# Kernel optimization log

Measured on AMD Instinct MI355X. Metric: run time of the kernel, lower is better.

Reference implementation:

```python
import jax, jax.numpy as jnp
import numpy as np

B, T, S, D, H, FF = 4, 1024, 1024, 1024, 16, 4096
DH = D // H
NEG = -1e9
EPS = 1e-5


def setup_inputs() -> dict:
    key = jax.random.key(0)
    ks = jax.random.split(key, 20)
    p = 0.02  # param init scale
    inp = {
        "x": jax.random.normal(ks[0], (B, T, D), jnp.float32),
        "encoder_output": jax.random.normal(ks[1], (B, S, D), jnp.float32),
        "src_mask": jnp.ones((B, 1, 1, S), jnp.bool_),
        "tgt_mask": jnp.tril(jnp.ones((1, 1, T, T), jnp.bool_)),  # causal
        # self-attention params
        "d_Wq": jax.random.normal(ks[2], (D, D)) * p, "d_bq": jnp.zeros((D,)),
        "d_Wk": jax.random.normal(ks[3], (D, D)) * p, "d_bk": jnp.zeros((D,)),
        "d_Wv": jax.random.normal(ks[4], (D, D)) * p, "d_bv": jnp.zeros((D,)),
        "d_Wo": jax.random.normal(ks[5], (D, D)) * p, "d_bo": jnp.zeros((D,)),
        # cross-attention params
        "e_Wq": jax.random.normal(ks[6], (D, D)) * p, "e_bq": jnp.zeros((D,)),
        "e_Wk": jax.random.normal(ks[7], (D, D)) * p, "e_bk": jnp.zeros((D,)),
        "e_Wv": jax.random.normal(ks[8], (D, D)) * p, "e_bv": jnp.zeros((D,)),
        "e_Wo": jax.random.normal(ks[9], (D, D)) * p, "e_bo": jnp.zeros((D,)),
        # FFN params
        "ff_W1": jax.random.normal(ks[10], (D, FF)) * p, "ff_b1": jnp.zeros((FF,)),
        "ff_W2": jax.random.normal(ks[11], (FF, D)) * p, "ff_b2": jnp.zeros((D,)),
        # layernorm params
        "ln1_g": jnp.ones((D,)), "ln1_b": jnp.zeros((D,)),
        "ln2_g": jnp.ones((D,)), "ln2_b": jnp.zeros((D,)),
        "ln3_g": jnp.ones((D,)), "ln3_b": jnp.zeros((D,)),
    }
    return inp


def _mha(xq, xkv, Wq, bq, Wk, bk, Wv, bv, Wo, bo, mask):
    b, tq = xq.shape[0], xq.shape[1]
    q = (xq @ Wq + bq).reshape(b, tq, H, DH).transpose(0, 2, 1, 3)
    k = (xkv @ Wk + bk).reshape(b, -1, H, DH).transpose(0, 2, 1, 3)
    v = (xkv @ Wv + bv).reshape(b, -1, H, DH).transpose(0, 2, 1, 3)
    scores = jnp.einsum("bhqd,bhkd->bhqk", q, k) / np.float32(np.sqrt(DH))
    scores = jnp.where(mask, scores, NEG)
    attn = jax.nn.softmax(scores, axis=-1)
    out = jnp.einsum("bhqk,bhkd->bhqd", attn, v)
    out = out.transpose(0, 2, 1, 3).reshape(b, tq, D)
    return out @ Wo + bo


def _ln(x, g, b):
    m = jnp.mean(x, axis=-1, keepdims=True)
    v = jnp.var(x, axis=-1, keepdims=True)
    return (x - m) / jnp.sqrt(v + EPS) * g + b


def reference(x, encoder_output, src_mask, tgt_mask,
              d_Wq, d_bq, d_Wk, d_bk, d_Wv, d_bv, d_Wo, d_bo,
              e_Wq, e_bq, e_Wk, e_bk, e_Wv, e_bv, e_Wo, e_bo,
              ff_W1, ff_b1, ff_W2, ff_b2,
              ln1_g, ln1_b, ln2_g, ln2_b, ln3_g, ln3_b):
    # masked self-attention + residual + LN (dropout is identity in eval)
    d = _mha(x, x, d_Wq, d_bq, d_Wk, d_bk, d_Wv, d_bv, d_Wo, d_bo, tgt_mask)
    d = _ln(d + x, ln1_g, ln1_b)
    # cross-attention over encoder output + residual + LN
    f = _mha(d, encoder_output, e_Wq, e_bq, e_Wk, e_bk, e_Wv, e_bv, e_Wo, e_bo, src_mask)
    f = _ln(f + d, ln2_g, ln2_b)
    # FFN + residual + LN
    g = jax.nn.relu(f @ ff_W1 + ff_b1) @ ff_W2 + ff_b2
    g = _ln(g + f, ln3_g, ln3_b)
    return g
```

## Files before the change

kernel.cpp:

```cpp
#include <hip/hip_runtime.h>

static constexpr int Bc = 4, Tc = 1024, Sc = 1024, Dc = 1024, Hc = 16, DHc = 64, FFc = 4096;

typedef __attribute__((ext_vector_type(8))) short short8;
typedef __attribute__((ext_vector_type(4))) short short4v;
typedef __attribute__((ext_vector_type(4))) float f32x4;

__device__ __forceinline__ unsigned short f2bf(float f) {
    unsigned int u = __float_as_uint(f);
    unsigned int r = u + 0x7fffu + ((u >> 16) & 1u);
    return (unsigned short)(r >> 16);
}
__device__ __forceinline__ float bf2f(unsigned short u) {
    return __uint_as_float(((unsigned int)u) << 16);
}
__device__ __forceinline__ float fexp2(float x) {
    float r; asm("v_exp_f32 %0, %1" : "=v"(r) : "v"(x)); return r;
}
__device__ __forceinline__ unsigned int cvtpk(float a, float b) {
    unsigned int r;
    asm("v_cvt_pk_bf16_f32 %0, %1, %2" : "=v"(r) : "v"(a), "v"(b));
    return r;
}

__device__ __forceinline__ void gload_lds16(const void* g, void* l) {
    __builtin_amdgcn_global_load_lds((const __attribute__((address_space(1))) void*)g,
                                     (__attribute__((address_space(3))) void*)l, 16, 0, 0);
}

__global__ __launch_bounds__(256) void cast_f32_bf16(const float* __restrict__ in,
                                                     unsigned short* __restrict__ out, int n8) {
    int i = blockIdx.x * 256 + threadIdx.x;
    if (i >= n8) return;
    const float4* p = (const float4*)in + (size_t)i * 2;
    float4 a = p[0], b = p[1];
    short8 o;
    o[0] = f2bf(a.x); o[1] = f2bf(a.y); o[2] = f2bf(a.z); o[3] = f2bf(a.w);
    o[4] = f2bf(b.x); o[5] = f2bf(b.y); o[6] = f2bf(b.z); o[7] = f2bf(b.w);
    *(short8*)(out + (size_t)i * 8) = o;
}

__global__ __launch_bounds__(256) void transpose_cast(const float* __restrict__ W,
                                                      unsigned short* __restrict__ Wt,
                                                      int K, int N) {
    __shared__ float tile[32][33];
    int n0 = blockIdx.x * 32, k0 = blockIdx.y * 32;
    int tx = threadIdx.x, ty = threadIdx.y;
#pragma unroll
    for (int i = 0; i < 4; i++)
        tile[ty + i * 8][tx] = W[(size_t)(k0 + ty + i * 8) * N + n0 + tx];
    __syncthreads();
#pragma unroll
    for (int i = 0; i < 4; i++)
        Wt[(size_t)(n0 + ty + i * 8) * K + k0 + tx] = f2bf(tile[tx][ty + i * 8]);
}

struct TP8 { const float* s[8]; unsigned short* d[8]; };
__global__ __launch_bounds__(256) void transpose_cast8(TP8 p) {
    __shared__ float tile[32][33];
    const float* W = p.s[blockIdx.z];
    unsigned short* Wt = p.d[blockIdx.z];
    int n0 = blockIdx.x * 32, k0 = blockIdx.y * 32;
    int tx = threadIdx.x, ty = threadIdx.y;
#pragma unroll
    for (int i = 0; i < 4; i++)
        tile[ty + i * 8][tx] = W[(size_t)(k0 + ty + i * 8) * 1024 + n0 + tx];
    __syncthreads();
#pragma unroll
    for (int i = 0; i < 4; i++)
        Wt[(size_t)(n0 + ty + i * 8) * 1024 + k0 + tx] = f2bf(tile[tx][ty + i * 8]);
}

__global__ void concat_bias(const float* b0, const float* b1, const float* b2,
                            float* __restrict__ out) {
    int i = blockIdx.x * 256 + threadIdx.x;
    int seg = i >> 10, j = i & 1023;
    const float* p = seg == 0 ? b0 : (seg == 1 ? b1 : b2);
    out[i] = p[j];
}

__global__ __launch_bounds__(256) void transpose_v(const unsigned short* __restrict__ V, int ldv,
                                                   unsigned short* __restrict__ Vt) {
    __shared__ unsigned short t[64 * 64];
    const int bh = blockIdx.y, b = bh >> 4, h = bh & 15;
    const int s0 = blockIdx.x * 64;
    const int tid = threadIdx.x;
    const int r = tid >> 2, ch = tid & 3;
    const unsigned short* src = V + (size_t)(b * 1024 + s0 + r) * ldv + h * 64 + ch * 16;
    short8 v0 = *(const short8*)src;
    short8 v1 = *(const short8*)(src + 8);
    int pw_ = (ch ^ r ^ (r >> 4)) & 3;
    *(short8*)(t + r * 64 + pw_ * 16) = v0;
    *(short8*)(t + r * 64 + pw_ * 16 + 8) = v1;
    __syncthreads();
    const int dh = tid >> 2, sc = (tid & 3) * 16;
    short8 o0, o1;
#pragma unroll
    for (int j = 0; j < 8; j++) {
        int c0 = sc + j, c1 = sc + 8 + j;
        o0[j] = t[c0 * 64 + (((dh >> 4) ^ c0 ^ (c0 >> 4)) & 3) * 16 + (dh & 15)];
        o1[j] = t[c1 * 64 + (((dh >> 4) ^ c1 ^ (c1 >> 4)) & 3) * 16 + (dh & 15)];
    }
    unsigned short* dst = Vt + ((size_t)bh * 64 + dh) * 1024 + s0 + sc;
    *(short8*)dst = o0;
    *(short8*)(dst + 8) = o1;
}

struct BlkMap { int m, n, z; };
__device__ __forceinline__ BlkMap remap_block() {
    const int gx = gridDim.x, gy = gridDim.y;
    const int nxy = gx * gy;
    const int nwg = nxy * gridDim.z;
    const int flat = (blockIdx.z * gy + blockIdx.y) * gx + blockIdx.x;
    const int id = (flat & 7) * (nwg >> 3) + (flat >> 3);
    const int pz = id / nxy;
    const int rz = id - pz * nxy;
    const int gwsh = (gx & 7) ? 2 : 3;
    const int gw = 1 << gwsh;
    const int gsz = gw * gy;
    const int grp = rz / gsz;
    const int rem = rz - grp * gsz;
    BlkMap r;
    r.m = rem >> gwsh;
    r.n = (grp << gwsh) + (rem & (gw - 1));
    r.z = pz;
    return r;
}

template <int EPI>
__global__ __launch_bounds__(512, 2) void gemm256(const unsigned short* __restrict__ A,
                                                  const unsigned short* __restrict__ Bt,
                                                  const float* __restrict__ bias,
                                                  unsigned short* __restrict__ outB,
                                                  int N, int lda, int ldb, int nk) {
    __shared__ unsigned short sm[4][16384];
    const int tid = threadIdx.x;
    const int lane = tid & 63, wid = tid >> 6;
    const int l4 = lane & 15, g = lane >> 4;
    const int wr = wid >> 2, wc = wid & 3;
    BlkMap bm = remap_block();
    const int m0 = bm.m * 256, n0 = bm.n * 256, z = bm.z;
    A += (size_t)z * (nk * 64);
    Bt += (size_t)z * (nk * 64);
    const int srow = tid >> 3;
    const int schunk = (tid & 7) ^ (srow & 7);
    const int sw = l4 & 7;

    auto stA = [&](int sb, int seg, int k0) {
        gload_lds16(A + (size_t)(m0 + seg * 64 + srow) * lda + k0 + schunk * 8,
                    (char*)sm[sb] + seg * 8192 + tid * 16);
    };
    auto stB = [&](int sb, int seg, int k0) {
        gload_lds16(Bt + (size_t)(n0 + seg * 64 + srow) * ldb + k0 + schunk * 8,
                    (char*)sm[2 + sb] + seg * 8192 + tid * 16);
    };

    f32x4 acc[8][4] = {};
#pragma unroll
    for (int s = 0; s < 4; s++) stB(0, s, 0);
#pragma unroll
    for (int s = 0; s < 4; s++) stA(0, s, 0);
    asm volatile("s_waitcnt vmcnt(0)" ::: "memory");
    __builtin_amdgcn_s_barrier();

    for (int t = 0; t < nk; ++t) {
        const int bufR = t & 1, bufW = bufR ^ 1;
        const int kn = (t + 1) * 64;
        const bool pf = (t + 1 < nk);
        const unsigned short* As_ = sm[bufR];
        const unsigned short* Bs_ = sm[2 + bufR];
        short8 a[4], b0[4], b1[4];
        if (pf) { stB(bufW, 0, kn); stB(bufW, 1, kn); }
#pragma unroll
        for (int n = 0; n < 4; n++)
            b0[n] = *(const short8*)(Bs_ + (wc * 64 + n * 16 + l4) * 64 + (g ^ sw) * 8);
#pragma unroll
        for (int m = 0; m < 4; m++)
            a[m] = *(const short8*)(As_ + (wr * 128 + m * 16 + l4) * 64 + (g ^ sw) * 8);
        __builtin_amdgcn_s_barrier();
        __builtin_amdgcn_s_setprio(1);
#pragma unroll
        for (int m = 0; m < 4; m++)
#pragma unroll
            for (int n = 0; n < 4; n++)
                acc[m][n] = __builtin_amdgcn_mfma_f32_16x16x32_bf16(a[m], b0[n], acc[m][n], 0, 0, 0);
        __builtin_amdgcn_s_setprio(0);
        __builtin_amdgcn_s_barrier();
        if (pf) { stB(bufW, 2, kn); stB(bufW, 3, kn); }
#pragma unroll
        for (int n = 0; n < 4; n++)
            b1[n] = *(const short8*)(Bs_ + (wc * 64 + n * 16 + l4) * 64 + ((4 + g) ^ sw) * 8);
#pragma unroll
        for (int m = 0; m < 4; m++)
            a[m] = *(const short8*)(As_ + (wr * 128 + m * 16 + l4) * 64 + ((4 + g) ^ sw) * 8);
        __builtin_amdgcn_s_barrier();
        __builtin_amdgcn_s_setprio(1);
#pragma unroll
        for (int m = 0; m < 4; m++)
#pragma unroll
            for (int n = 0; n < 4; n++)
                acc[m][n] = __builtin_amdgcn_mfma_f32_16x16x32_bf16(a[m], b1[n], acc[m][n], 0, 0, 0);
        __builtin_amdgcn_s_setprio(0);
        if (pf) asm volatile("s_waitcnt vmcnt(4)" ::: "memory");
        else    asm volatile("s_waitcnt vmcnt(0)" ::: "memory");
        __builtin_amdgcn_s_barrier();
        if (pf) { stA(bufW, 0, kn); stA(bufW, 2, kn); }
#pragma unroll
        for (int m = 0; m < 4; m++)
            a[m] = *(const short8*)(As_ + (wr * 128 + 64 + m * 16 + l4) * 64 + (g ^ sw) * 8);
        __builtin_amdgcn_s_barrier();
        __builtin_amdgcn_s_setprio(1);
#pragma unroll
        for (int m = 0; m < 4; m++)
#pragma unroll
            for (int n = 0; n < 4; n++)
                acc[4 + m][n] = __builtin_amdgcn_mfma_f32_16x16x32_bf16(a[m], b0[n], acc[4 + m][n], 0, 0, 0);
        __builtin_amdgcn_s_setprio(0);
        __builtin_amdgcn_s_barrier();
        if (pf) { stA(bufW, 1, kn); stA(bufW, 3, kn); }
#pragma unroll
        for (int m = 0; m < 4; m++)
            a[m] = *(const short8*)(As_ + (wr * 128 + 64 + m * 16 + l4) * 64 + ((4 + g) ^ sw) * 8);
        __builtin_amdgcn_s_barrier();
        __builtin_amdgcn_s_setprio(1);
#pragma unroll
        for (int m = 0; m < 4; m++)
#pragma unroll
            for (int n = 0; n < 4; n++)
                acc[4 + m][n] = __builtin_amdgcn_mfma_f32_16x16x32_bf16(a[m], b1[n], acc[4 + m][n], 0, 0, 0);
        __builtin_amdgcn_s_setprio(0);
        if (pf) asm volatile("s_waitcnt vmcnt(2)" ::: "memory");
        __builtin_amdgcn_s_barrier();
    }
    unsigned short* eb = (unsigned short*)sm;
    unsigned short* oB = outB;
    if (EPI == 3) oB += (size_t)z * ((size_t)gridDim.y * 256) * N;
    const int colL = wc * 64 + l4;
#pragma unroll
    for (int h = 0; h < 2; ++h) {
        if (wr == h) {
#pragma unroll
            for (int mm = 0; mm < 8; mm++) {
                const int base_r = (mm < 4 ? mm * 16 : 64 + (mm - 4) * 16) + g * 4;
#pragma unroll
                for (int n = 0; n < 4; n++) {
                    float bv = (EPI == 3 && z != 0) ? 0.f : bias[n0 + colL + n * 16];
#pragma unroll
                    for (int r = 0; r < 4; r++) {
                        float v = acc[mm][n][r] + bv;
                        if (EPI == 2) v = fmaxf(v, 0.f);
                        eb[(base_r + r) * 260 + colL + n * 16] = f2bf(v);
                    }
                }
            }
        }
        __syncthreads();
        const int gr0 = m0 + h * 128;
#pragma unroll
        for (int j = 0; j < 8; j++) {
            const int f = j * 8192 + tid * 16;
            const int row = f >> 9;
            const int colb = f & 511;
            short8 v = *(const short8*)((const char*)eb + row * 520 + colb);
            *(short8*)(oB + (size_t)(gr0 + row) * N + n0 + (colb >> 1)) = v;
        }
        if (h == 0) __syncthreads();
    }
}

template <int EPI>
__global__ __launch_bounds__(256) void gemm64_db(const unsigned short* __restrict__ A,
                                                 const unsigned short* __restrict__ Bt,
                                                 const float* __restrict__ bias,
                                                 float* __restrict__ outF,
                                                 unsigned short* __restrict__ outB,
                                                 int M, int N, int Kloop, int lda, int ldb) {
    __shared__ unsigned short As[3][64 * 32];
    __shared__ unsigned short Bs[3][128 * 32];
    const int tid = threadIdx.x;
    const int w = tid >> 6, lane = tid & 63, l4 = lane & 15, g = lane >> 4;
    BlkMap bm = remap_block();
    const int m0 = bm.m * 64, n0 = bm.n * 128;
    f32x4 acc[4][2] = {};
    const int r0 = tid >> 2;
    const int kk = ((tid & 3) ^ ((tid >> 3) & 3)) * 8;
    const int sk = (l4 >> 1) & 3;
    const unsigned short* Ar0 = A + (size_t)(m0 + r0) * lda + kk;
    const unsigned short* Br0 = Bt + (size_t)(n0 + r0) * ldb + kk;
    const unsigned short* Br1 = Bt + (size_t)(n0 + 64 + r0) * ldb + kk;
    auto stage = [&](int sb, int k0) {
        gload_lds16(Ar0 + k0, (char*)As[sb] + tid * 16);
        gload_lds16(Br0 + k0, (char*)Bs[sb] + tid * 16);
        gload_lds16(Br1 + k0, (char*)Bs[sb] + 4096 + tid * 16);
    };
    const int nk = Kloop >> 5;
    stage(0, 0);
    stage(1, 32);
    asm volatile("s_waitcnt vmcnt(3)" ::: "memory");
    __builtin_amdgcn_s_barrier();
    asm volatile("" ::: "memory");
    int buf = 0;
    for (int t = 0; t < nk; ++t) {
        if (t + 2 < nk) {
            int b2 = buf + 2; if (b2 >= 3) b2 -= 3;
            stage(b2, (t + 2) * 32);
        }
        short8 a[4], b[2];
#pragma unroll
        for (int m = 0; m < 4; m++)
            a[m] = *(const short8*)(As[buf] + (m * 16 + l4) * 32 + (g ^ sk) * 8);
#pragma unroll
        for (int n = 0; n < 2; n++)
            b[n] = *(const short8*)(Bs[buf] + (w * 32 + n * 16 + l4) * 32 + (g ^ sk) * 8);
#pragma unroll
        for (int m = 0; m < 4; m++)
#pragma unroll
            for (int n = 0; n < 2; n++)
                acc[m][n] = __builtin_amdgcn_mfma_f32_16x16x32_bf16(a[m], b[n], acc[m][n], 0, 0, 0);
        if (t + 1 < nk) {
            if (t + 2 < nk) asm volatile("s_waitcnt vmcnt(3)" ::: "memory");
            else            asm volatile("s_waitcnt vmcnt(0)" ::: "memory");
            __builtin_amdgcn_s_barrier();
            asm volatile("" ::: "memory");
        }
        buf = (buf + 1 == 3) ? 0 : buf + 1;
    }
    const int rowB = m0 + g * 4;
    const int colB = n0 + w * 32 + l4;
#pragma unroll
    for (int n = 0; n < 2; n++) {
        float bv = bias[colB + n * 16];
#pragma unroll
        for (int m = 0; m < 4; m++) {
#pragma unroll
            for (int r = 0; r < 4; r++) {
                float v = acc[m][n][r] + bv;
                if (EPI == 2) v = fmaxf(v, 0.f);
                size_t idx = (size_t)(rowB + m * 16 + r) * N + colB + n * 16;
                if (EPI == 1) outF[idx] = v;
                else outB[idx] = f2bf(v);
            }
        }
    }
}

template <int CAUSAL>
__global__ __launch_bounds__(256) void attn5_kernel(const unsigned short* __restrict__ Q, int ldq,
                                                    const unsigned short* __restrict__ Kg, int ldk,
                                                    const unsigned short* __restrict__ Vt,
                                                    unsigned short* __restrict__ O) {
    __shared__ unsigned short Kl[2 * 64 * 64];
    __shared__ unsigned short Vl[2 * 64 * 64];
    __shared__ unsigned short Pl[4][16 * 72];
    const int bh = blockIdx.x;
    const int qb = CAUSAL ? (gridDim.y - 1 - blockIdx.y) : blockIdx.y;
    const int b = bh >> 4, h = bh & 15;
    const int tid = threadIdx.x, w = tid >> 6, lane = tid & 63;
    const int l4 = lane & 15, g = lane >> 4;
    const int q0 = qb * 64 + w * 16;
    const unsigned short* Qp = Q + (size_t)(b * Tc + q0 + l4) * ldq + h * DHc + g * 8;
    short8 qf0 = *(const short8*)Qp;
    short8 qf1 = *(const short8*)(Qp + 32);
    const unsigned short* Kbase = Kg + (size_t)(b * 1024) * ldk + h * DHc;
    const unsigned short* Vbase = Vt + (size_t)bh * DHc * 1024;
    f32x4 o[4] = {};
    float mrun = -1e30f, lrun = 0.f;
    const int nT = CAUSAL ? qb + 1 : 16;
    unsigned short* pw = &Pl[w][l4 * 72];
    const int qi = q0 + l4;
    constexpr float SC = 0.125f * 1.44269504f;

    short8 ones;
#pragma unroll
    for (int j = 0; j < 8; j++) ones[j] = (short)0x3F80;

    const int sr0 = tid >> 3;
    const int sr1 = 32 + sr0;
    const int sc_ = (tid & 7) ^ (sr0 & 7);

    auto stage = [&](int s0, int buf) {
        char* kd = (char*)Kl + buf * 8192;
        char* vd = (char*)Vl + buf * 8192;
        gload_lds16(Kbase + (size_t)(s0 + sr0) * ldk + sc_ * 8, kd + tid * 16);
        gload_lds16(Kbase + (size_t)(s0 + sr1) * ldk + sc_ * 8, kd + 4096 + tid * 16);
        gload_lds16(Vbase + (size_t)sr0 * 1024 + s0 + sc_ * 8, vd + tid * 16);
        gload_lds16(Vbase + (size_t)sr1 * 1024 + s0 + sc_ * 8, vd + 4096 + tid * 16);
    };

    stage(0, 0);
    __syncthreads();
    int buf = 0;
    const int sw = l4 & 7;

    for (int t = 0; t < nT; ++t) {
        const int s0 = t * 64;
        if (t + 1 < nT) stage(s0 + 64, buf ^ 1);
        const unsigned short* Kb_ = Kl + buf * 4096;
        const unsigned short* Vb_ = Vl + buf * 4096;
        f32x4 st[4];
        f32x4 z = {0.f, 0.f, 0.f, 0.f};
        __builtin_amdgcn_s_setprio(1);
#pragma unroll
        for (int c = 0; c < 4; c++) {
            const unsigned short* kr = Kb_ + (c * 16 + l4) * 64;
            short8 ka0 = *(const short8*)(kr + ((g ^ sw) * 8));
            short8 ka1 = *(const short8*)(kr + (((g + 4) ^ sw) * 8));
            st[c] = __builtin_amdgcn_mfma_f32_16x16x32_bf16(ka0, qf0, z, 0, 0, 0);
            st[c] = __builtin_amdgcn_mfma_f32_16x16x32_bf16(ka1, qf1, st[c], 0, 0, 0);
        }
        __builtin_amdgcn_s_setprio(0);
        float p[16];
        const bool domask = CAUSAL && (t == nT - 1);
#pragma unroll
        for (int c = 0; c < 4; c++)
#pragma unroll
            for (int r = 0; r < 4; r++) {
                float v = st[c][r] * SC;
                if (domask && (s0 + c * 16 + g * 4 + r) > qi) v = -1e9f;
                p[c * 4 + r] = v;
            }
        float m1 = fmaxf(fmaxf(p[0], p[1]), p[2]);
        float m2 = fmaxf(fmaxf(p[3], p[4]), p[5]);
        float m3 = fmaxf(fmaxf(p[6], p[7]), p[8]);
        float m4 = fmaxf(fmaxf(p[9], p[10]), p[11]);
        float m5 = fmaxf(fmaxf(p[12], p[13]), p[14]);
        float tmax = fmaxf(fmaxf(fmaxf(m1, m2), fmaxf(m3, m4)), fmaxf(m5, p[15]));
        tmax = fmaxf(tmax, __shfl_xor(tmax, 16));
        tmax = fmaxf(tmax, __shfl_xor(tmax, 32));
        if (!__all(tmax <= mrun + 11.5f)) {
            float mnew = fmaxf(mrun, tmax);
            float al = fexp2(mrun - mnew);
            lrun *= al;
#pragma unroll
            for (int d = 0; d < 4; d++) o[d] *= al;
            mrun = mnew;
        }
#pragma unroll
        for (int i = 0; i < 16; i++) p[i] = fexp2(p[i] - mrun);
#pragma unroll
        for (int c = 0; c < 4; c++) {
            uint2 u;
            u.x = cvtpk(p[c * 4 + 0], p[c * 4 + 1]);
            u.y = cvtpk(p[c * 4 + 2], p[c * 4 + 3]);
            *(uint2*)(pw + c * 16 + g * 4) = u;
        }
        short8 pb_lo = *(const short8*)(pw + g * 8);
        short8 pb_hi = *(const short8*)(pw + 32 + g * 8);
        __builtin_amdgcn_s_setprio(1);
        f32x4 s4 = __builtin_amdgcn_mfma_f32_16x16x32_bf16(ones, pb_lo, z, 0, 0, 0);
        s4 = __builtin_amdgcn_mfma_f32_16x16x32_bf16(ones, pb_hi, s4, 0, 0, 0);
#pragma unroll
        for (int d = 0; d < 4; d++) {
            const unsigned short* vr = Vb_ + (d * 16 + l4) * 64;
            short8 va0 = *(const short8*)(vr + ((g ^ sw) * 8));
            short8 va1 = *(const short8*)(vr + (((g + 4) ^ sw) * 8));
            o[d] = __builtin_amdgcn_mfma_f32_16x16x32_bf16(va0, pb_lo, o[d], 0, 0, 0);
            o[d] = __builtin_amdgcn_mfma_f32_16x16x32_bf16(va1, pb_hi, o[d], 0, 0, 0);
        }
        __builtin_amdgcn_s_setprio(0);
        lrun += s4[0];
        __syncthreads();
        buf ^= 1;
    }
    float inv = 1.f / lrun;
    unsigned short* Ob = O + (size_t)(b * Tc + q0 + l4) * Dc + h * DHc;
#pragma unroll
    for (int d = 0; d < 4; d++) {
#pragma unroll
        for (int r = 0; r < 4; r++) Ob[d * 16 + g * 4 + r] = f2bf(o[d][r] * inv);
    }
}

__global__ __launch_bounds__(256) void ln_bf(const unsigned short* __restrict__ a,
                                             const unsigned short* __restrict__ res,
                                             const float* __restrict__ gam,
                                             const float* __restrict__ bet,
                                             unsigned short* __restrict__ outB,
                                             float* __restrict__ outF) {
    int row = blockIdx.x, t = threadIdx.x;
    size_t base = (size_t)row * Dc + t * 4;
    short4v av = *(const short4v*)(a + base);
    short4v rv = *(const short4v*)(res + base);
    float x0 = bf2f((unsigned short)av[0]) + bf2f((unsigned short)rv[0]);
    float x1 = bf2f((unsigned short)av[1]) + bf2f((unsigned short)rv[1]);
    float x2 = bf2f((unsigned short)av[2]) + bf2f((unsigned short)rv[2]);
    float x3 = bf2f((unsigned short)av[3]) + bf2f((unsigned short)rv[3]);
    float s = x0 + x1 + x2 + x3;
    float ss = x0 * x0 + x1 * x1 + x2 * x2 + x3 * x3;
    for (int o = 1; o < 64; o <<= 1) { s += __shfl_xor(s, o); ss += __shfl_xor(ss, o); }
    __shared__ float S1[4], S2[4];
    int w = t >> 6;
    if ((t & 63) == 0) { S1[w] = s; S2[w] = ss; }
    __syncthreads();
    s = S1[0] + S1[1] + S1[2] + S1[3];
    ss = S2[0] + S2[1] + S2[2] + S2[3];
    float mean = s * (1.f / Dc);
    float var = ss * (1.f / Dc) - mean * mean;
    float rstd = rsqrtf(var + 1e-5f);
    int c = t * 4;
    float4 g4 = *(const float4*)(gam + c);
    float4 b4 = *(const float4*)(bet + c);
    float y0 = (x0 - mean) * rstd * g4.x + b4.x;
    float y1 = (x1 - mean) * rstd * g4.y + b4.y;
    float y2 = (x2 - mean) * rstd * g4.z + b4.z;
    float y3 = (x3 - mean) * rstd * g4.w + b4.w;
    if (outB) {
        short4v ob;
        ob[0] = f2bf(y0); ob[1] = f2bf(y1); ob[2] = f2bf(y2); ob[3] = f2bf(y3);
        *(short4v*)(outB + base) = ob;
    }
    if (outF) { float4 ov = {y0, y1, y2, y3}; *(float4*)(outF + base) = ov; }
}

__global__ __launch_bounds__(256) void ln_4b(const unsigned short* __restrict__ p,
                                             const unsigned short* __restrict__ res,
                                             const float* __restrict__ gam,
                                             const float* __restrict__ bet,
                                             float* __restrict__ outF) {
    const size_t PS = (size_t)4096 * 1024;
    int row = blockIdx.x, t = threadIdx.x;
    size_t base = (size_t)row * Dc + t * 4;
    float x0, x1, x2, x3;
    {
        short4v rv = *(const short4v*)(res + base);
        x0 = bf2f((unsigned short)rv[0]); x1 = bf2f((unsigned short)rv[1]);
        x2 = bf2f((unsigned short)rv[2]); x3 = bf2f((unsigned short)rv[3]);
    }
#pragma unroll
    for (int j = 0; j < 4; j++) {
        short4v v = *(const short4v*)(p + j * PS + base);
        x0 += bf2f((unsigned short)v[0]); x1 += bf2f((unsigned short)v[1]);
        x2 += bf2f((unsigned short)v[2]); x3 += bf2f((unsigned short)v[3]);
    }
    float s = x0 + x1 + x2 + x3;
    float ss = x0 * x0 + x1 * x1 + x2 * x2 + x3 * x3;
    for (int o = 1; o < 64; o <<= 1) { s += __shfl_xor(s, o); ss += __shfl_xor(ss, o); }
    __shared__ float S1[4], S2[4];
    int w = t >> 6;
    if ((t & 63) == 0) { S1[w] = s; S2[w] = ss; }
    __syncthreads();
    s = S1[0] + S1[1] + S1[2] + S1[3];
    ss = S2[0] + S2[1] + S2[2] + S2[3];
    float mean = s * (1.f / Dc);
    float var = ss * (1.f / Dc) - mean * mean;
    float rstd = rsqrtf(var + 1e-5f);
    int c = t * 4;
    float4 g4 = *(const float4*)(gam + c);
    float4 b4 = *(const float4*)(bet + c);
    float4 ov;
    ov.x = (x0 - mean) * rstd * g4.x + b4.x;
    ov.y = (x1 - mean) * rstd * g4.y + b4.y;
    ov.z = (x2 - mean) * rstd * g4.z + b4.z;
    ov.w = (x3 - mean) * rstd * g4.w + b4.w;
    *(float4*)(outF + base) = ov;
}

extern "C" void kernel_launch(void* const* d_in, const int* in_sizes, int n_in,
                              void* d_out, int out_size, void* d_ws, size_t ws_size,
                              hipStream_t stream) {
    const float* x   = (const float*)d_in[0];
    const float* enc = (const float*)d_in[1];
    const float* dWq = (const float*)d_in[4];  const float* dbq = (const float*)d_in[5];
    const float* dWk = (const float*)d_in[6];  const float* dbk = (const float*)d_in[7];
    const float* dWv = (const float*)d_in[8];  const float* dbv = (const float*)d_in[9];
    const float* dWo = (const float*)d_in[10]; const float* dbo = (const float*)d_in[11];
    const float* eWq = (const float*)d_in[12]; const float* ebq = (const float*)d_in[13];
    const float* eWk = (const float*)d_in[14]; const float* ebk = (const float*)d_in[15];
    const float* eWv = (const float*)d_in[16]; const float* ebv = (const float*)d_in[17];
    const float* eWo = (const float*)d_in[18]; const float* ebo = (const float*)d_in[19];
    const float* fW1 = (const float*)d_in[20]; const float* fb1 = (const float*)d_in[21];
    const float* fW2 = (const float*)d_in[22]; const float* fb2 = (const float*)d_in[23];
    const float* g1 = (const float*)d_in[24];  const float* be1 = (const float*)d_in[25];
    const float* g2 = (const float*)d_in[26];  const float* be2 = (const float*)d_in[27];
    const float* g3 = (const float*)d_in[28];  const float* be3 = (const float*)d_in[29];

    char* ws = (char*)d_ws;
    size_t off = 0;
    auto alloc = [&](size_t bytes) -> void* {
        void* p = ws + off;
        off += (bytes + 255) & ~(size_t)255;
        return p;
    };
    const size_t A = (size_t)4096 * 1024;
    const size_t MB1 = (size_t)1024 * 1024;
    char* R1 = (char*)alloc(32 * 1024 * 1024);
    unsigned short* qkv = (unsigned short*)R1;
    unsigned short* kvx = (unsigned short*)R1;
    unsigned short* qx  = (unsigned short*)(R1 + 16 * 1024 * 1024);
    unsigned short* h1  = (unsigned short*)R1;
    unsigned short* xb   = (unsigned short*)alloc(A * 2);
    unsigned short* encb = (unsigned short*)alloc(A * 2);
    unsigned short* wqkv = (unsigned short*)alloc(3 * MB1 * 2);
    unsigned short* wekv = (unsigned short*)alloc(2 * MB1 * 2);
    unsigned short* weq  = (unsigned short*)alloc(MB1 * 2);
    unsigned short* wdo  = (unsigned short*)alloc(MB1 * 2);
    unsigned short* weo  = (unsigned short*)alloc(MB1 * 2);
    unsigned short* wf1  = (unsigned short*)alloc(4 * MB1 * 2);
    unsigned short* wf2  = (unsigned short*)alloc(4 * MB1 * 2);
    float* bqkv = (float*)alloc(3072 * 4);
    float* bekv = (float*)alloc(2048 * 4);
    unsigned short* VtB = (unsigned short*)alloc(A * 2);
    unsigned short* ab  = (unsigned short*)alloc(A * 2);
    unsigned short* tmpB = (unsigned short*)alloc(A * 2);
    unsigned short* dB = (unsigned short*)alloc(A * 2);
    unsigned short* fB = (unsigned short*)alloc(A * 2);
    unsigned short* pfb = VtB;
    (void)ws_size; (void)in_sizes; (void)n_in; (void)out_size;

    dim3 tb(32, 8);
    cast_f32_bf16<<<2048, 256, 0, stream>>>(x, xb, (int)(A / 8));
    cast_f32_bf16<<<2048, 256, 0, stream>>>(enc, encb, (int)(A / 8));
    TP8 tp;
    tp.s[0] = dWq; tp.d[0] = wqkv;
    tp.s[1] = dWk; tp.d[1] = wqkv + MB1;
    tp.s[2] = dWv; tp.d[2] = wqkv + 2 * MB1;
    tp.s[3] = eWk; tp.d[3] = wekv;
    tp.s[4] = eWv; tp.d[4] = wekv + MB1;
    tp.s[5] = eWq; tp.d[5] = weq;
    tp.s[6] = dWo; tp.d[6] = wdo;
    tp.s[7] = eWo; tp.d[7] = weo;
    transpose_cast8<<<dim3(32, 32, 8), tb, 0, stream>>>(tp);
    transpose_cast<<<dim3(128, 32), tb, 0, stream>>>(fW1, wf1, 1024, 4096);
    transpose_cast<<<dim3(32, 128), tb, 0, stream>>>(fW2, wf2, 4096, 1024);
    concat_bias<<<12, 256, 0, stream>>>(dbq, dbk, dbv, bqkv);
    concat_bias<<<8, 256, 0, stream>>>(ebk, ebv, ebv, bekv);

    gemm256<0><<<dim3(12, 16), 512, 0, stream>>>(xb, wqkv, bqkv, qkv, 3072, 1024, 1024, 16);
    transpose_v<<<dim3(16, 64), 256, 0, stream>>>(qkv + 2048, 3072, VtB);
    attn5_kernel<1><<<dim3(64, 16), 256, 0, stream>>>(qkv, 3072, qkv + 1024, 3072, VtB, ab);
    gemm64_db<0><<<dim3(8, 64), 256, 0, stream>>>(ab, wdo, dbo, nullptr, tmpB, 4096, 1024, 1024, 1024, 1024);
    ln_bf<<<4096, 256, 0, stream>>>(tmpB, xb, g1, be1, dB, nullptr);

    gemm256<0><<<dim3(8, 16), 512, 0, stream>>>(encb, wekv, bekv, kvx, 2048, 1024, 1024, 16);
    gemm64_db<0><<<dim3(8, 64), 256, 0, stream>>>(dB, weq, ebq, nullptr, qx, 4096, 1024, 1024, 1024, 1024);
    transpose_v<<<dim3(16, 64), 256, 0, stream>>>(kvx + 1024, 2048, VtB);
    attn5_kernel<0><<<dim3(64, 16), 256, 0, stream>>>(qx, 1024, kvx, 2048, VtB, ab);
    gemm64_db<0><<<dim3(8, 64), 256, 0, stream>>>(ab, weo, ebo, nullptr, tmpB, 4096, 1024, 1024, 1024, 1024);
    ln_bf<<<4096, 256, 0, stream>>>(tmpB, dB, g2, be2, fB, nullptr);

    gemm256<2><<<dim3(16, 16), 512, 0, stream>>>(fB, wf1, fb1, h1, 4096, 1024, 1024, 16);
    gemm256<3><<<dim3(4, 16, 4), 512, 0, stream>>>(h1, wf2, fb2, pfb, 1024, 4096, 4096, 16);
    ln_4b<<<4096, 256, 0, stream>>>(pfb, fB, g3, be3, (float*)d_out);
}
```

Measured before the change: 349.2 us.

## Fold softmax scale into Q weights and widen attention blocks to 128 queries

```diff
diff --git a/kernel.cpp b/kernel.cpp
--- a/kernel.cpp
+++ b/kernel.cpp
@@ -55,11 +55,12 @@
         Wt[(size_t)(n0 + ty + i * 8) * K + k0 + tx] = f2bf(tile[tx][ty + i * 8]);
 }
 
-struct TP8 { const float* s[8]; unsigned short* d[8]; };
+struct TP8 { const float* s[8]; unsigned short* d[8]; float scl[8]; };
 __global__ __launch_bounds__(256) void transpose_cast8(TP8 p) {
     __shared__ float tile[32][33];
     const float* W = p.s[blockIdx.z];
     unsigned short* Wt = p.d[blockIdx.z];
+    const float sc = p.scl[blockIdx.z];
     int n0 = blockIdx.x * 32, k0 = blockIdx.y * 32;
     int tx = threadIdx.x, ty = threadIdx.y;
 #pragma unroll
@@ -68,15 +69,16 @@
     __syncthreads();
 #pragma unroll
     for (int i = 0; i < 4; i++)
-        Wt[(size_t)(n0 + ty + i * 8) * 1024 + k0 + tx] = f2bf(tile[tx][ty + i * 8]);
+        Wt[(size_t)(n0 + ty + i * 8) * 1024 + k0 + tx] = f2bf(tile[tx][ty + i * 8] * sc);
 }
 
 __global__ void concat_bias(const float* b0, const float* b1, const float* b2,
-                            float* __restrict__ out) {
+                            float s0, float s1, float s2, float* __restrict__ out) {
     int i = blockIdx.x * 256 + threadIdx.x;
     int seg = i >> 10, j = i & 1023;
     const float* p = seg == 0 ? b0 : (seg == 1 ? b1 : b2);
-    out[i] = p[j];
+    float sc = seg == 0 ? s0 : (seg == 1 ? s1 : s2);
+    out[i] = p[j] * sc;
 }
 
 __global__ __launch_bounds__(256) void transpose_v(const unsigned short* __restrict__ V, int ldv,
@@ -345,19 +347,19 @@
 }
 
 template <int CAUSAL>
-__global__ __launch_bounds__(256) void attn5_kernel(const unsigned short* __restrict__ Q, int ldq,
+__global__ __launch_bounds__(512) void attn6_kernel(const unsigned short* __restrict__ Q, int ldq,
                                                     const unsigned short* __restrict__ Kg, int ldk,
                                                     const unsigned short* __restrict__ Vt,
                                                     unsigned short* __restrict__ O) {
     __shared__ unsigned short Kl[2 * 64 * 64];
     __shared__ unsigned short Vl[2 * 64 * 64];
-    __shared__ unsigned short Pl[4][16 * 72];
+    __shared__ unsigned short Pl[8][16 * 72];
     const int bh = blockIdx.x;
     const int qb = CAUSAL ? (gridDim.y - 1 - blockIdx.y) : blockIdx.y;
     const int b = bh >> 4, h = bh & 15;
     const int tid = threadIdx.x, w = tid >> 6, lane = tid & 63;
     const int l4 = lane & 15, g = lane >> 4;
-    const int q0 = qb * 64 + w * 16;
+    const int q0 = qb * 128 + w * 16;
     const unsigned short* Qp = Q + (size_t)(b * Tc + q0 + l4) * ldq + h * DHc + g * 8;
     short8 qf0 = *(const short8*)Qp;
     short8 qf1 = *(const short8*)(Qp + 32);
@@ -365,26 +367,22 @@
     const unsigned short* Vbase = Vt + (size_t)bh * DHc * 1024;
     f32x4 o[4] = {};
     float mrun = -1e30f, lrun = 0.f;
-    const int nT = CAUSAL ? qb + 1 : 16;
+    const int nT = CAUSAL ? 2 * qb + 2 : 16;
     unsigned short* pw = &Pl[w][l4 * 72];
     const int qi = q0 + l4;
-    constexpr float SC = 0.125f * 1.44269504f;
 
     short8 ones;
 #pragma unroll
     for (int j = 0; j < 8; j++) ones[j] = (short)0x3F80;
 
-    const int sr0 = tid >> 3;
-    const int sr1 = 32 + sr0;
-    const int sc_ = (tid & 7) ^ (sr0 & 7);
+    const int sr = tid >> 3;
+    const int sc_ = (tid & 7) ^ (sr & 7);
 
     auto stage = [&](int s0, int buf) {
         char* kd = (char*)Kl + buf * 8192;
         char* vd = (char*)Vl + buf * 8192;
-        gload_lds16(Kbase + (size_t)(s0 + sr0) * ldk + sc_ * 8, kd + tid * 16);
-        gload_lds16(Kbase + (size_t)(s0 + sr1) * ldk + sc_ * 8, kd + 4096 + tid * 16);
-        gload_lds16(Vbase + (size_t)sr0 * 1024 + s0 + sc_ * 8, vd + tid * 16);
-        gload_lds16(Vbase + (size_t)sr1 * 1024 + s0 + sc_ * 8, vd + 4096 + tid * 16);
+        gload_lds16(Kbase + (size_t)(s0 + sr) * ldk + sc_ * 8, kd + tid * 16);
+        gload_lds16(Vbase + (size_t)sr * 1024 + s0 + sc_ * 8, vd + tid * 16);
     };
 
     stage(0, 0);
@@ -395,70 +393,72 @@
     for (int t = 0; t < nT; ++t) {
         const int s0 = t * 64;
         if (t + 1 < nT) stage(s0 + 64, buf ^ 1);
-        const unsigned short* Kb_ = Kl + buf * 4096;
-        const unsigned short* Vb_ = Vl + buf * 4096;
-        f32x4 st[4];
-        f32x4 z = {0.f, 0.f, 0.f, 0.f};
-        __builtin_amdgcn_s_setprio(1);
-#pragma unroll
-        for (int c = 0; c < 4; c++) {
-            const unsigned short* kr = Kb_ + (c * 16 + l4) * 64;
-            short8 ka0 = *(const short8*)(kr + ((g ^ sw) * 8));
-            short8 ka1 = *(const short8*)(kr + (((g + 4) ^ sw) * 8));
-            st[c] = __builtin_amdgcn_mfma_f32_16x16x32_bf16(ka0, qf0, z, 0, 0, 0);
-            st[c] = __builtin_amdgcn_mfma_f32_16x16x32_bf16(ka1, qf1, st[c], 0, 0, 0);
+        if (!CAUSAL || s0 <= q0 + 15) {
+            const unsigned short* Kb_ = Kl + buf * 4096;
+            const unsigned short* Vb_ = Vl + buf * 4096;
+            f32x4 st[4];
+            f32x4 z = {0.f, 0.f, 0.f, 0.f};
+            __builtin_amdgcn_s_setprio(1);
+#pragma unroll
+            for (int c = 0; c < 4; c++) {
+                const unsigned short* kr = Kb_ + (c * 16 + l4) * 64;
+                short8 ka0 = *(const short8*)(kr + ((g ^ sw) * 8));
+                short8 ka1 = *(const short8*)(kr + (((g + 4) ^ sw) * 8));
+                st[c] = __builtin_amdgcn_mfma_f32_16x16x32_bf16(ka0, qf0, z, 0, 0, 0);
+                st[c] = __builtin_amdgcn_mfma_f32_16x16x32_bf16(ka1, qf1, st[c], 0, 0, 0);
+            }
+            __builtin_amdgcn_s_setprio(0);
+            float p[16];
+            const bool domask = CAUSAL && (s0 + 63 > q0);
+#pragma unroll
+            for (int c = 0; c < 4; c++)
+#pragma unroll
+                for (int r = 0; r < 4; r++) {
+                    float v = st[c][r];
+                    if (domask && (s0 + c * 16 + g * 4 + r) > qi) v = -1e9f;
+                    p[c * 4 + r] = v;
+                }
+            float m1 = fmaxf(fmaxf(p[0], p[1]), p[2]);
+            float m2 = fmaxf(fmaxf(p[3], p[4]), p[5]);
+            float m3 = fmaxf(fmaxf(p[6], p[7]), p[8]);
+            float m4 = fmaxf(fmaxf(p[9], p[10]), p[11]);
+            float m5 = fmaxf(fmaxf(p[12], p[13]), p[14]);
+            float tmax = fmaxf(fmaxf(fmaxf(m1, m2), fmaxf(m3, m4)), fmaxf(m5, p[15]));
+            tmax = fmaxf(tmax, __shfl_xor(tmax, 16));
+            tmax = fmaxf(tmax, __shfl_xor(tmax, 32));
+            if (!__all(tmax <= mrun + 11.5f)) {
+                float mnew = fmaxf(mrun, tmax);
+                float al = fexp2(mrun - mnew);
+                lrun *= al;
+#pragma unroll
+                for (int d = 0; d < 4; d++) o[d] *= al;
+                mrun = mnew;
+            }
+#pragma unroll
+            for (int i = 0; i < 16; i++) p[i] = fexp2(p[i] - mrun);
+#pragma unroll
+            for (int c = 0; c < 4; c++) {
+                uint2 u;
+                u.x = cvtpk(p[c * 4 + 0], p[c * 4 + 1]);
+                u.y = cvtpk(p[c * 4 + 2], p[c * 4 + 3]);
+                *(uint2*)(pw + c * 16 + g * 4) = u;
+            }
+            short8 pb_lo = *(const short8*)(pw + g * 8);
+            short8 pb_hi = *(const short8*)(pw + 32 + g * 8);
+            __builtin_amdgcn_s_setprio(1);
+            f32x4 s4 = __builtin_amdgcn_mfma_f32_16x16x32_bf16(ones, pb_lo, z, 0, 0, 0);
+            s4 = __builtin_amdgcn_mfma_f32_16x16x32_bf16(ones, pb_hi, s4, 0, 0, 0);
+#pragma unroll
+            for (int d = 0; d < 4; d++) {
+                const unsigned short* vr = Vb_ + (d * 16 + l4) * 64;
+                short8 va0 = *(const short8*)(vr + ((g ^ sw) * 8));
+                short8 va1 = *(const short8*)(vr + (((g + 4) ^ sw) * 8));
+                o[d] = __builtin_amdgcn_mfma_f32_16x16x32_bf16(va0, pb_lo, o[d], 0, 0, 0);
+                o[d] = __builtin_amdgcn_mfma_f32_16x16x32_bf16(va1, pb_hi, o[d], 0, 0, 0);
+            }
+            __builtin_amdgcn_s_setprio(0);
+            lrun += s4[0];
         }
-        __builtin_amdgcn_s_setprio(0);
-        float p[16];
-        const bool domask = CAUSAL && (t == nT - 1);
-#pragma unroll
-        for (int c = 0; c < 4; c++)
-#pragma unroll
-            for (int r = 0; r < 4; r++) {
-                float v = st[c][r] * SC;
-                if (domask && (s0 + c * 16 + g * 4 + r) > qi) v = -1e9f;
-                p[c * 4 + r] = v;
-            }
-        float m1 = fmaxf(fmaxf(p[0], p[1]), p[2]);
-        float m2 = fmaxf(fmaxf(p[3], p[4]), p[5]);
-        float m3 = fmaxf(fmaxf(p[6], p[7]), p[8]);
-        float m4 = fmaxf(fmaxf(p[9], p[10]), p[11]);
-        float m5 = fmaxf(fmaxf(p[12], p[13]), p[14]);
-        float tmax = fmaxf(fmaxf(fmaxf(m1, m2), fmaxf(m3, m4)), fmaxf(m5, p[15]));
-        tmax = fmaxf(tmax, __shfl_xor(tmax, 16));
-        tmax = fmaxf(tmax, __shfl_xor(tmax, 32));
-        if (!__all(tmax <= mrun + 11.5f)) {
-            float mnew = fmaxf(mrun, tmax);
-            float al = fexp2(mrun - mnew);
-            lrun *= al;
-#pragma unroll
-            for (int d = 0; d < 4; d++) o[d] *= al;
-            mrun = mnew;
-        }
-#pragma unroll
-        for (int i = 0; i < 16; i++) p[i] = fexp2(p[i] - mrun);
-#pragma unroll
-        for (int c = 0; c < 4; c++) {
-            uint2 u;
-            u.x = cvtpk(p[c * 4 + 0], p[c * 4 + 1]);
-            u.y = cvtpk(p[c * 4 + 2], p[c * 4 + 3]);
-            *(uint2*)(pw + c * 16 + g * 4) = u;
-        }
-        short8 pb_lo = *(const short8*)(pw + g * 8);
-        short8 pb_hi = *(const short8*)(pw + 32 + g * 8);
-        __builtin_amdgcn_s_setprio(1);
-        f32x4 s4 = __builtin_amdgcn_mfma_f32_16x16x32_bf16(ones, pb_lo, z, 0, 0, 0);
-        s4 = __builtin_amdgcn_mfma_f32_16x16x32_bf16(ones, pb_hi, s4, 0, 0, 0);
-#pragma unroll
-        for (int d = 0; d < 4; d++) {
-            const unsigned short* vr = Vb_ + (d * 16 + l4) * 64;
-            short8 va0 = *(const short8*)(vr + ((g ^ sw) * 8));
-            short8 va1 = *(const short8*)(vr + (((g + 4) ^ sw) * 8));
-            o[d] = __builtin_amdgcn_mfma_f32_16x16x32_bf16(va0, pb_lo, o[d], 0, 0, 0);
-            o[d] = __builtin_amdgcn_mfma_f32_16x16x32_bf16(va1, pb_hi, o[d], 0, 0, 0);
-        }
-        __builtin_amdgcn_s_setprio(0);
-        lrun += s4[0];
         __syncthreads();
         buf ^= 1;
     }
@@ -574,6 +574,8 @@
     const float* g2 = (const float*)d_in[26];  const float* be2 = (const float*)d_in[27];
     const float* g3 = (const float*)d_in[28];  const float* be3 = (const float*)d_in[29];
 
+    const float SC = 0.125f * 1.44269504f;
+
     char* ws = (char*)d_ws;
     size_t off = 0;
     auto alloc = [&](size_t bytes) -> void* {
@@ -599,6 +601,7 @@
     unsigned short* wf2  = (unsigned short*)alloc(4 * MB1 * 2);
     float* bqkv = (float*)alloc(3072 * 4);
     float* bekv = (float*)alloc(2048 * 4);
+    float* ebq_s = (float*)alloc(1024 * 4);
     unsigned short* VtB = (unsigned short*)alloc(A * 2);
     unsigned short* ab  = (unsigned short*)alloc(A * 2);
     unsigned short* tmpB = (unsigned short*)alloc(A * 2);
@@ -611,30 +614,31 @@
     cast_f32_bf16<<<2048, 256, 0, stream>>>(x, xb, (int)(A / 8));
     cast_f32_bf16<<<2048, 256, 0, stream>>>(enc, encb, (int)(A / 8));
     TP8 tp;
-    tp.s[0] = dWq; tp.d[0] = wqkv;
-    tp.s[1] = dWk; tp.d[1] = wqkv + MB1;
-    tp.s[2] = dWv; tp.d[2] = wqkv + 2 * MB1;
-    tp.s[3] = eWk; tp.d[3] = wekv;
-    tp.s[4] = eWv; tp.d[4] = wekv + MB1;
-    tp.s[5] = eWq; tp.d[5] = weq;
-    tp.s[6] = dWo; tp.d[6] = wdo;
-    tp.s[7] = eWo; tp.d[7] = weo;
+    tp.s[0] = dWq; tp.d[0] = wqkv;           tp.scl[0] = SC;
+    tp.s[1] = dWk; tp.d[1] = wqkv + MB1;     tp.scl[1] = 1.f;
+    tp.s[2] = dWv; tp.d[2] = wqkv + 2 * MB1; tp.scl[2] = 1.f;
+    tp.s[3] = eWk; tp.d[3] = wekv;           tp.scl[3] = 1.f;
+    tp.s[4] = eWv; tp.d[4] = wekv + MB1;     tp.scl[4] = 1.f;
+    tp.s[5] = eWq; tp.d[5] = weq;            tp.scl[5] = SC;
+    tp.s[6] = dWo; tp.d[6] = wdo;            tp.scl[6] = 1.f;
+    tp.s[7] = eWo; tp.d[7] = weo;            tp.scl[7] = 1.f;
     transpose_cast8<<<dim3(32, 32, 8), tb, 0, stream>>>(tp);
     transpose_cast<<<dim3(128, 32), tb, 0, stream>>>(fW1, wf1, 1024, 4096);
     transpose_cast<<<dim3(32, 128), tb, 0, stream>>>(fW2, wf2, 4096, 1024);
-    concat_bias<<<12, 256, 0, stream>>>(dbq, dbk, dbv, bqkv);
-    concat_bias<<<8, 256, 0, stream>>>(ebk, ebv, ebv, bekv);
+    concat_bias<<<12, 256, 0, stream>>>(dbq, dbk, dbv, SC, 1.f, 1.f, bqkv);
+    concat_bias<<<8, 256, 0, stream>>>(ebk, ebv, ebv, 1.f, 1.f, 1.f, bekv);
+    concat_bias<<<4, 256, 0, stream>>>(ebq, ebq, ebq, SC, SC, SC, ebq_s);
 
     gemm256<0><<<dim3(12, 16), 512, 0, stream>>>(xb, wqkv, bqkv, qkv, 3072, 1024, 1024, 16);
     transpose_v<<<dim3(16, 64), 256, 0, stream>>>(qkv + 2048, 3072, VtB);
-    attn5_kernel<1><<<dim3(64, 16), 256, 0, stream>>>(qkv, 3072, qkv + 1024, 3072, VtB, ab);
+    attn6_kernel<1><<<dim3(64, 8), 512, 0, stream>>>(qkv, 3072, qkv + 1024, 3072, VtB, ab);
     gemm64_db<0><<<dim3(8, 64), 256, 0, stream>>>(ab, wdo, dbo, nullptr, tmpB, 4096, 1024, 1024, 1024, 1024);
     ln_bf<<<4096, 256, 0, stream>>>(tmpB, xb, g1, be1, dB, nullptr);
 
     gemm256<0><<<dim3(8, 16), 512, 0, stream>>>(encb, wekv, bekv, kvx, 2048, 1024, 1024, 16);
-    gemm64_db<0><<<dim3(8, 64), 256, 0, stream>>>(dB, weq, ebq, nullptr, qx, 4096, 1024, 1024, 1024, 1024);
+    gemm64_db<0><<<dim3(8, 64), 256, 0, stream>>>(dB, weq, ebq_s, nullptr, qx, 4096, 1024, 1024, 1024, 1024);
     transpose_v<<<dim3(16, 64), 256, 0, stream>>>(kvx + 1024, 2048, VtB);
-    attn5_kernel<0><<<dim3(64, 16), 256, 0, stream>>>(qx, 1024, kvx, 2048, VtB, ab);
+    attn6_kernel<0><<<dim3(64, 8), 512, 0, stream>>>(qx, 1024, kvx, 2048, VtB, ab);
     gemm64_db<0><<<dim3(8, 64), 256, 0, stream>>>(ab, weo, ebo, nullptr, tmpB, 4096, 1024, 1024, 1024, 1024);
     ln_bf<<<4096, 256, 0, stream>>>(tmpB, dB, g2, be2, fB, nullptr);
 
```

Result: faster. 336.6 us (-3.6%).
